# Optimization experiments

Hardware: AMD Instinct MI355X
Metric: run time of the kernel (lower is better)

The kernel has to match this reference:

```python
import jax, jax.numpy as jnp
import numpy as np

N = 200000
MESH = (128, 128, 128)   # mesh_dimensions
P = 4                    # spline_order
ALPHA = 0.35             # Ewald splitting parameter (1/Angstrom)
KE = 14.3996             # coulomb_constant, eV*A/e^2
BOX = 128.0              # cubic box edge, Angstrom


def _bspline(u, n):
    """Cardinal B-spline M_n(u), support [0, n]. Recursion depth = n-2 (static)."""
    if n == 2:
        return jnp.clip(1.0 - jnp.abs(u - 1.0), 0.0, 1.0)
    return (u * _bspline(u, n - 1) + (n - u) * _bspline(u - 1.0, n - 1)) / (n - 1)


def _spread_weights(frac_d, K):
    """Per-dimension P spline weights and wrapped grid indices for each atom."""
    u = frac_d * K
    base = jnp.floor(u)
    j = jnp.arange(P, dtype=frac_d.dtype)
    # evaluation points t_j = (u - base) + (P-1) - j, each in (0, P)
    t = (u - base)[:, None] + (P - 1) - j                      # [N, P]
    w = _bspline(t, P)                                         # [N, P]
    idx = (base.astype(jnp.int32)[:, None] - (P - 1)
           + jnp.arange(P, dtype=jnp.int32)) % K               # [N, P]
    return w, idx


def _bmod2(K):
    """|b(m)|^2 Euler exponential-spline factors for one mesh dimension."""
    m = (jnp.fft.fftfreq(K) * K).astype(jnp.float32)
    k = jnp.arange(P - 1, dtype=jnp.float32)
    Mv = _bspline(k + 1.0, P)                                  # M_P(1..P-1)
    D = (Mv[None, :] * jnp.exp(2j * jnp.pi * m[:, None] * k[None, :] / K)).sum(-1)
    return (1.0 / jnp.maximum(jnp.abs(D) ** 2, 1e-12)).astype(jnp.float32)


def _pme_energy(positions, charges, cell):
    Kx, Ky, Kz = MESH
    cellinv = jnp.linalg.inv(cell)
    V = jnp.abs(jnp.linalg.det(cell))
    frac = (positions @ cellinv) % 1.0                         # [N, 3]

    # --- B-spline charge spreading (scatter) ---
    wx, ix = _spread_weights(frac[:, 0], Kx)
    wy, iy = _spread_weights(frac[:, 1], Ky)
    wz, iz = _spread_weights(frac[:, 2], Kz)
    w3 = (charges[:, None, None, None]
          * wx[:, :, None, None] * wy[:, None, :, None] * wz[:, None, None, :])
    lin = (ix[:, :, None, None] * Ky + iy[:, None, :, None]) * Kz + iz[:, None, None, :]
    Q = (jnp.zeros(Kx * Ky * Kz, dtype=positions.dtype)
         .at[lin.reshape(-1)].add(w3.reshape(-1))
         .reshape(MESH))

    # --- reciprocal space ---
    S = jnp.fft.fftn(Q)
    S2 = (S * jnp.conj(S)).real                                # |F[Q]|^2
    b3 = (_bmod2(Kx)[:, None, None] * _bmod2(Ky)[None, :, None]
          * _bmod2(Kz)[None, None, :])
    mx = (jnp.fft.fftfreq(Kx) * Kx).astype(positions.dtype)
    my = (jnp.fft.fftfreq(Ky) * Ky).astype(positions.dtype)
    mz = (jnp.fft.fftfreq(Kz) * Kz).astype(positions.dtype)
    mg = jnp.stack(jnp.meshgrid(mx, my, mz, indexing='ij'), axis=-1)  # [Kx,Ky,Kz,3]
    kvec = 2.0 * jnp.pi * jnp.einsum('xyzm,nm->xyzn', mg, cellinv)
    k2 = (kvec ** 2).sum(-1)
    G = jnp.where(k2 > 0.0,
                  jnp.exp(-k2 / (4.0 * ALPHA ** 2)) / jnp.where(k2 > 0.0, k2, 1.0),
                  0.0)
    e_rec = KE * (2.0 * jnp.pi / V) * (G * b3 * S2).sum()
    e_self = -KE * ALPHA / jnp.sqrt(jnp.pi).astype(positions.dtype) * (charges ** 2).sum()
    return e_rec + e_self


def setup_inputs() -> dict:
    key = jax.random.key(0)
    k1, k2 = jax.random.split(key)
    positions = jax.random.uniform(k1, (N, 3), dtype=jnp.float32) * BOX
    charges = jax.random.normal(k2, (N,), dtype=jnp.float32) * 0.5
    charges = charges - charges.mean()   # neutral system (k=0 mode excluded)
    cell = jnp.eye(3, dtype=jnp.float32) * BOX
    return {"positions": positions, "charges": charges, "cell": cell}


def reference(positions, charges, cell):
    # energy [B=1, 1] and analytic forces [N, 3] via force gather (dE/dr)
    e, g = jax.value_and_grad(lambda p: _pme_energy(p, charges, cell))(positions)
    return (jnp.reshape(e, (1, 1)), -g)
```

## Files before the change

kernel.cpp:

```cpp
#include <hip/hip_runtime.h>

#define KDIM 128
#define NTOT (KDIM * KDIM * KDIM)
#define BPD 16
#define NBINS (BPD * BPD * BPD)
#define TILE_D 11
#define T2 (TILE_D * TILE_D)
#define TILE_N (TILE_D * TILE_D * TILE_D)
#define TPAD 1332
#define TSTRIDE 1344
#define CHUNK 256
#define NZKEEP 65
#define NSCALE_BLK (NZKEEP * 8)
#define ST 17
#define ZST 17

static constexpr float PI_F = 3.14159265358979323846f;
static constexpr float TWO_PI_F = 6.28318530717958647692f;
static constexpr float KE_F = 14.3996f;
static constexpr float ALPHA_F = 0.35f;

__device__ __forceinline__ int brev7(int i) { return (int)(__brev((unsigned)i) >> 25); }

__device__ __forceinline__ void inv3x3(const float* c, float* inv, float* adet) {
    float a00 = c[0], a01 = c[1], a02 = c[2];
    float a10 = c[3], a11 = c[4], a12 = c[5];
    float a20 = c[6], a21 = c[7], a22 = c[8];
    float det = a00 * (a11 * a22 - a12 * a21) - a01 * (a10 * a22 - a12 * a20) +
                a02 * (a10 * a21 - a11 * a20);
    float id = 1.0f / det;
    inv[0] = (a11 * a22 - a12 * a21) * id;
    inv[1] = (a02 * a21 - a01 * a22) * id;
    inv[2] = (a01 * a12 - a02 * a11) * id;
    inv[3] = (a12 * a20 - a10 * a22) * id;
    inv[4] = (a00 * a22 - a02 * a20) * id;
    inv[5] = (a02 * a10 - a00 * a12) * id;
    inv[6] = (a10 * a21 - a11 * a20) * id;
    inv[7] = (a01 * a20 - a00 * a21) * id;
    inv[8] = (a00 * a11 - a01 * a10) * id;
    *adet = fabsf(det);
}

__device__ __forceinline__ void bspline4(float f, float* w, float* dw) {
    float f2 = f * f, f3 = f2 * f;
    float omf = 1.0f - f;
    w[0] = omf * omf * omf * (1.0f / 6.0f);
    w[1] = (3.0f * f3 - 6.0f * f2 + 4.0f) * (1.0f / 6.0f);
    w[2] = (-3.0f * f3 + 3.0f * f2 + 3.0f * f + 1.0f) * (1.0f / 6.0f);
    w[3] = f3 * (1.0f / 6.0f);
    dw[0] = -0.5f * omf * omf;
    dw[1] = 1.5f * f2 - 2.0f * f;
    dw[2] = -1.5f * f2 + f + 0.5f;
    dw[3] = 0.5f * f2;
}

__device__ __forceinline__ void atom_base(const float* __restrict__ pos, const float* inv,
                                          int i, int base[3], float fpart[3]) {
    float p0 = pos[3 * i], p1 = pos[3 * i + 1], p2 = pos[3 * i + 2];
#pragma unroll
    for (int d = 0; d < 3; d++) {
        float fr = p0 * inv[d] + p1 * inv[3 + d] + p2 * inv[6 + d];
        fr -= floorf(fr);
        float u = fr * (float)KDIM;
        float bs = floorf(u);
        fpart[d] = u - bs;
        int b = (int)bs;
        base[d] = b & (KDIM - 1);
    }
}

__device__ __forceinline__ void atom_setup(const float* __restrict__ pos, const float* inv,
                                           int i, float wgt[3][4], float dwg[3][4],
                                           int idx[3][4]) {
    int base[3];
    float fp[3];
    atom_base(pos, inv, i, base, fp);
#pragma unroll
    for (int d = 0; d < 3; d++) {
        bspline4(fp[d], wgt[d], dwg[d]);
#pragma unroll
        for (int j = 0; j < 4; j++) idx[d][j] = (base[d] - 3 + j + KDIM) & (KDIM - 1);
    }
}

__device__ __forceinline__ float bmod2f(int x) {
    float th = (TWO_PI_F / (float)KDIM) * (float)x;
    float s1, c1, s2, c2;
    __sincosf(th, &s1, &c1);
    __sincosf(th + th, &s2, &c2);
    float dr = 0.16666667f + 0.66666667f * c1 + 0.16666667f * c2;
    float di = 0.66666667f * s1 + 0.16666667f * s2;
    float d2 = dr * dr + di * di;
    return 1.0f / fmaxf(d2, 1e-12f);
}

__global__ __launch_bounds__(256) void zero_tbl_kernel(int* __restrict__ counts,
                                                       int* __restrict__ cursor,
                                                       float* __restrict__ mtblS,
                                                       float* __restrict__ btblS) {
    int i = blockIdx.x * 256 + threadIdx.x;
    if (i < NBINS) {
        counts[i] = 0;
        cursor[i] = 0;
    }
    if (blockIdx.x == 0 && threadIdx.x < KDIM) {
        int r = brev7(threadIdx.x);
        mtblS[threadIdx.x] = (float)(r < 64 ? r : r - 128);
        btblS[threadIdx.x] = bmod2f(r);
    }
}

__global__ __launch_bounds__(256) void hist_kernel(const float* __restrict__ pos,
                                                   const float* __restrict__ chg,
                                                   const float* __restrict__ cell,
                                                   int* __restrict__ counts,
                                                   float* __restrict__ q2_part, int n) {
    __shared__ float hred[4];
    int i = blockIdx.x * blockDim.x + threadIdx.x;
    float q2 = 0.0f;
    if (i < n) {
        float inv[9], det;
        inv3x3(cell, inv, &det);
        int base[3];
        float fp[3];
        atom_base(pos, inv, i, base, fp);
        int bid = ((base[0] >> 3) << 8) | ((base[1] >> 3) << 4) | (base[2] >> 3);
        atomicAdd(&counts[bid], 1);
        float qi = chg[i];
        q2 = qi * qi;
    }
#pragma unroll
    for (int off = 32; off; off >>= 1) q2 += __shfl_down(q2, off);
    if ((threadIdx.x & 63) == 0) hred[threadIdx.x >> 6] = q2;
    __syncthreads();
    if (threadIdx.x == 0) q2_part[blockIdx.x] = hred[0] + hred[1] + hred[2] + hred[3];
}

__global__ __launch_bounds__(256) void scan_kernel(const int* __restrict__ counts,
                                                   int* __restrict__ starts) {
    __shared__ int part[256];
    int tid = threadIdx.x;
    int local[NBINS / 256];
    int sum = 0;
#pragma unroll
    for (int k = 0; k < NBINS / 256; k++) {
        local[k] = counts[tid * (NBINS / 256) + k];
        sum += local[k];
    }
    part[tid] = sum;
    __syncthreads();
    if (tid == 0) {
        int acc = 0;
        for (int i = 0; i < 256; i++) {
            int t = part[i];
            part[i] = acc;
            acc += t;
        }
        starts[NBINS] = acc;
    }
    __syncthreads();
    int acc = part[tid];
#pragma unroll
    for (int k = 0; k < NBINS / 256; k++) {
        starts[tid * (NBINS / 256) + k] = acc;
        acc += local[k];
    }
}

__global__ __launch_bounds__(256) void scatter_kernel(const float* __restrict__ pos,
                                                      const float* __restrict__ chg,
                                                      const float* __restrict__ cell,
                                                      const int* __restrict__ starts,
                                                      int* __restrict__ cursor,
                                                      float* __restrict__ records,
                                                      int* __restrict__ binatoms, int n) {
    int i = blockIdx.x * blockDim.x + threadIdx.x;
    if (i >= n) return;
    float inv[9], det;
    inv3x3(cell, inv, &det);
    int base[3];
    float fp[3];
    atom_base(pos, inv, i, base, fp);
    int bid = ((base[0] >> 3) << 8) | ((base[1] >> 3) << 4) | (base[2] >> 3);
    int slot = atomicAdd(&cursor[bid], 1) + starts[bid];
    binatoms[slot] = i;
    float4* rec = (float4*)(records + (size_t)slot * 16);
    float w[4], dw[4];
    float qi = chg[i];
    bspline4(fp[0], w, dw);
    rec[0] = make_float4(qi * w[0], qi * w[1], qi * w[2], qi * w[3]);
    bspline4(fp[1], w, dw);
    rec[1] = make_float4(w[0], w[1], w[2], w[3]);
    bspline4(fp[2], w, dw);
    rec[2] = make_float4(w[0], w[1], w[2], w[3]);
    int loc = (base[0] & 7) | ((base[1] & 7) << 4) | ((base[2] & 7) << 8);
    rec[3] = make_float4(__int_as_float(loc), 0.0f, 0.0f, 0.0f);
}

__global__ __launch_bounds__(256) void spread_bins_kernel(
    const float* __restrict__ records, const int* __restrict__ starts,
    float* __restrict__ tiles) {
    __shared__ float tile4[4 * TPAD];
    __shared__ float4 arec[CHUNK * 4];
    int tid = threadIdx.x;
    int bid = blockIdx.x;
    for (int i = tid; i < 4 * TPAD; i += 256) tile4[i] = 0.0f;
    int s = starts[bid], e = starts[bid + 1];
    int w = tid >> 6, l = tid & 63;
    int j0 = l >> 4, j1 = (l >> 2) & 3, j2 = l & 3;
    int joff = j0 * T2 + j1 * TILE_D + j2;
    float* mytile = tile4 + w * TPAD;
    for (int c0 = s; c0 < e; c0 += CHUNK) {
        int cnt = min(CHUNK, e - c0);
        __syncthreads();
        if (tid < cnt) {
            const float4* rp = (const float4*)records + (size_t)(c0 + tid) * 4;
            arec[tid * 4 + 0] = rp[0];
            arec[tid * 4 + 1] = rp[1];
            arec[tid * 4 + 2] = rp[2];
            arec[tid * 4 + 3] = rp[3];
        }
        __syncthreads();
        for (int a = w; a < cnt; a += 4) {
            const float* A = (const float*)&arec[a << 2];
            float val = A[j0] * A[4 + j1] * A[8 + j2];
            int lc = __float_as_int(A[12]);
            int tb = (lc & 15) * T2 + ((lc >> 4) & 15) * TILE_D + ((lc >> 8) & 15);
            mytile[tb + joff] += val;
        }
    }
    __syncthreads();
    float* tout = tiles + (size_t)bid * TSTRIDE;
    for (int i = tid; i < TILE_N; i += 256)
        tout[i] = tile4[i] + tile4[TPAD + i] + tile4[2 * TPAD + i] + tile4[3 * TPAD + i];
}

__device__ __forceinline__ float2 cmul(float2 a, float cs, float sn) {
    return make_float2(a.x * cs - a.y * sn, a.x * sn + a.y * cs);
}

__device__ __forceinline__ void wave_fft128_dif(float2& v0, float2& v1, int l, float sign) {
    {
        float ang = sign * (PI_F / 64.0f) * (float)l;
        float sn, cs;
        __sincosf(ang, &sn, &cs);
        float2 d = make_float2(v0.x - v1.x, v0.y - v1.y);
        v0 = make_float2(v0.x + v1.x, v0.y + v1.y);
        v1 = cmul(d, cs, sn);
    }
#pragma unroll
    for (int m = 32; m >= 1; m >>= 1) {
        float ang = sign * (PI_F / (float)m) * (float)(l & (m - 1));
        float sn, cs;
        __sincosf(ang, &sn, &cs);
        bool hi = (l & m) != 0;
        float2 p0, p1;
        p0.x = __shfl_xor(v0.x, m);
        p0.y = __shfl_xor(v0.y, m);
        p1.x = __shfl_xor(v1.x, m);
        p1.y = __shfl_xor(v1.y, m);
        float2 a0 = hi ? cmul(make_float2(p0.x - v0.x, p0.y - v0.y), cs, sn)
                       : make_float2(v0.x + p0.x, v0.y + p0.y);
        float2 a1 = hi ? cmul(make_float2(p1.x - v1.x, p1.y - v1.y), cs, sn)
                       : make_float2(v1.x + p1.x, v1.y + p1.y);
        v0 = a0;
        v1 = a1;
    }
}

__device__ __forceinline__ void wave_fft128_dit(float2& v0, float2& v1, int l, float sign) {
#pragma unroll
    for (int m = 1; m <= 32; m <<= 1) {
        float2 p0, p1;
        p0.x = __shfl_xor(v0.x, m);
        p0.y = __shfl_xor(v0.y, m);
        p1.x = __shfl_xor(v1.x, m);
        p1.y = __shfl_xor(v1.y, m);
        float ang = sign * (PI_F / (float)m) * (float)(l & (m - 1));
        float sn, cs;
        __sincosf(ang, &sn, &cs);
        bool hi = (l & m) != 0;
        float2 o0 = hi ? v0 : p0, e0 = hi ? p0 : v0;
        float2 o1 = hi ? v1 : p1, e1 = hi ? p1 : v1;
        float2 t0 = cmul(o0, cs, sn);
        float2 t1 = cmul(o1, cs, sn);
        float s = hi ? -1.0f : 1.0f;
        v0 = make_float2(e0.x + s * t0.x, e0.y + s * t0.y);
        v1 = make_float2(e1.x + s * t1.x, e1.y + s * t1.y);
    }
    float ang = sign * (PI_F / 64.0f) * (float)l;
    float sn, cs;
    __sincosf(ang, &sn, &cs);
    float2 t = cmul(v1, cs, sn);
    float2 e = v0;
    v0 = make_float2(e.x + t.x, e.y + t.y);
    v1 = make_float2(e.x - t.x, e.y - t.y);
}

__device__ __forceinline__ float merge_val(const float* __restrict__ tiles, int nx, int ny,
                                           const int* bxs, const int* lxs, const int* bys,
                                           const int* lys, int gz) {
    int bz = gz >> 3, oz = gz & 7;
    int nz = (oz >= 5) ? 2 : 1;
    int bzs[2] = {bz, (bz + 1) & 15}, lzs[2] = {oz + 3, oz - 5};
    float v = 0.0f;
    for (int i = 0; i < nx; i++)
        for (int j = 0; j < ny; j++) {
            int bxy = (bxs[i] << 8) | (bys[j] << 4);
            int lo = lxs[i] * T2 + lys[j] * TILE_D;
            for (int k = 0; k < nz; k++)
                v += tiles[(size_t)(bxy | bzs[k]) * TSTRIDE + lo + lzs[k]];
        }
    return v;
}

__global__ __launch_bounds__(512) void fft_z_merge(const float* __restrict__ tiles,
                                                   float2* __restrict__ C_t) {
    __shared__ float tr[128 * 9], ti[128 * 9];
    int w = threadIdx.x >> 6, l = threadIdx.x & 63;
    int line = (blockIdx.x << 3) + w;
    int gx = line >> 7, gy = line & 127;
    int bx = gx >> 3, ox = gx & 7;
    int by = gy >> 3, oy = gy & 7;
    int nx = (ox >= 5) ? 2 : 1, ny = (oy >= 5) ? 2 : 1;
    int bxs[2] = {bx, (bx + 1) & 15}, lxs[2] = {ox + 3, ox - 5};
    int bys[2] = {by, (by + 1) & 15}, lys[2] = {oy + 3, oy - 5};
    float m0 = merge_val(tiles, nx, ny, bxs, lxs, bys, lys, l);
    float m1 = merge_val(tiles, nx, ny, bxs, lxs, bys, lys, l + 64);
    tr[l * 9 + w] = m0;
    ti[l * 9 + w] = 0.0f;
    tr[(l + 64) * 9 + w] = m1;
    ti[(l + 64) * 9 + w] = 0.0f;
    int r = brev7(l);
    float2 v0 = make_float2(tr[r * 9 + w], 0.0f);
    float2 v1 = make_float2(tr[(r + 1) * 9 + w], 0.0f);
    wave_fft128_dit(v0, v1, l, -1.0f);
    tr[l * 9 + w] = v0.x;
    ti[l * 9 + w] = v0.y;
    tr[(l + 64) * 9 + w] = v1.x;
    ti[(l + 64) * 9 + w] = v1.y;
    __syncthreads();
    int xy0 = blockIdx.x << 3;
#pragma unroll
    for (int k = 0; k < 2; k++) {
        int e = threadIdx.x + (k << 9);
        int ss = e >> 3, wl = e & 7;
        if (ss < NZKEEP)
            C_t[(size_t)ss * (KDIM * KDIM) + xy0 + wl] =
                make_float2(tr[ss * 9 + wl], ti[ss * 9 + wl]);
    }
}

template <int DIF>
__global__ __launch_bounds__(512) void fft_y(float2* __restrict__ C_t) {
    int w = threadIdx.x >> 6, l = threadIdx.x & 63;
    int line = (blockIdx.x << 3) + w;
    int base = line << 7;
    float2 v0, v1;
    if (DIF) {
        v0 = C_t[base + l];
        v1 = C_t[base + l + 64];
        wave_fft128_dif(v0, v1, l, -1.0f);
    } else {
        int r = brev7(l);
        float4 f = ((const float4*)C_t)[(line << 6) + (r >> 1)];
        v0 = make_float2(f.x, f.y);
        v1 = make_float2(f.z, f.w);
        wave_fft128_dit(v0, v1, l, 1.0f);
    }
    C_t[base + l] = v0;
    C_t[base + l + 64] = v1;
}

__global__ __launch_bounds__(512) void fft_x_scale(float2* __restrict__ C_t,
                                                   const float* __restrict__ cell,
                                                   const float* __restrict__ mtblS,
                                                   const float* __restrict__ btblS,
                                                   float* __restrict__ scale_part) {
    __shared__ float2 lds[128 * ST];
    __shared__ float red[8];
    int tid = threadIdx.x;
    int s = blockIdx.x >> 3;
    int y0 = (blockIdx.x & 7) << 4;
    int base = s * (KDIM * KDIM) + y0;
#pragma unroll
    for (int k = 0; k < 2; k++) {
        int e = tid + (k << 9);
        int ll = e >> 3, zq = e & 7;
        float4 f = ((const float4*)C_t)[(base >> 1) + ll * 64 + zq];
        lds[ll * ST + 2 * zq] = make_float2(f.x, f.y);
        lds[ll * ST + 2 * zq + 1] = make_float2(f.z, f.w);
    }
    __syncthreads();
    int w = tid >> 6, l = tid & 63;
    float inv[9], det;
    inv3x3(cell, inv, &det);
    float mz = (s == 64) ? -64.0f : (float)s;
    float bz = bmod2f(s);
    float wz = (s == 0 || s == 64) ? 1.0f : 2.0f;
    float contrib = 0.0f;
#pragma unroll
    for (int c = 0; c < 2; c++) {
        int zt = (w << 1) | c;
        float2 v0 = lds[l * ST + zt];
        float2 v1 = lds[(l + 64) * ST + zt];
        wave_fft128_dif(v0, v1, l, -1.0f);
        int yp = y0 + zt;
        float my = mtblS[yp];
        float byz = btblS[yp] * bz;
#pragma unroll
        for (int h = 0; h < 2; h++) {
            int xs = l + (h << 6);
            float mx = mtblS[xs];
            float kx = TWO_PI_F * (mx * inv[0] + my * inv[1] + mz * inv[2]);
            float ky = TWO_PI_F * (mx * inv[3] + my * inv[4] + mz * inv[5]);
            float kz = TWO_PI_F * (mx * inv[6] + my * inv[7] + mz * inv[8]);
            float k2 = kx * kx + ky * ky + kz * kz;
            float A = 0.0f;
            if (k2 > 0.0f)
                A = __expf(-k2 / (4.0f * ALPHA_F * ALPHA_F)) / k2 * btblS[xs] * byz;
            float2& v = h ? v1 : v0;
            contrib += A * (v.x * v.x + v.y * v.y);
            v.x *= A;
            v.y *= A;
        }
        wave_fft128_dit(v0, v1, l, 1.0f);
        lds[l * ST + zt] = v0;
        lds[(l + 64) * ST + zt] = v1;
    }
    contrib *= wz;
#pragma unroll
    for (int off = 32; off; off >>= 1) contrib += __shfl_down(contrib, off);
    if (l == 0) red[w] = contrib;
    __syncthreads();
    if (tid == 0) {
        float v = 0.0f;
        for (int i = 0; i < 8; i++) v += red[i];
        scale_part[blockIdx.x] = v;
    }
#pragma unroll
    for (int k = 0; k < 2; k++) {
        int e = tid + (k << 9);
        int ll = e >> 3, zq = e & 7;
        float2 a = lds[ll * ST + 2 * zq];
        float2 b = lds[ll * ST + 2 * zq + 1];
        ((float4*)C_t)[(base >> 1) + ll * 64 + zq] = make_float4(a.x, a.y, b.x, b.y);
    }
}

__global__ __launch_bounds__(512) void fft_z_phi(const float2* __restrict__ C_t,
                                                 float* __restrict__ phi) {
    __shared__ float tr[NZKEEP * ZST], ti[NZKEEP * ZST];
    int tid = threadIdx.x;
    int xy0 = blockIdx.x << 4;
    for (int e = tid; e < NZKEEP * 16; e += 512) {
        int ss = e >> 4, q = e & 15;
        float2 v = C_t[(size_t)ss * (KDIM * KDIM) + xy0 + q];
        tr[ss * ZST + q] = v.x;
        ti[ss * ZST + q] = v.y;
    }
    __syncthreads();
    int w = tid >> 6, l = tid & 63;
    int r = brev7(l);
#pragma unroll
    for (int c0 = 0; c0 < 2; c0++) {
        int c = (w << 1) | c0;
        float2 v0, v1;
        if (r <= 62) {
            v0 = make_float2(tr[r * ZST + c], ti[r * ZST + c]);
            v1 = make_float2(tr[(r + 1) * ZST + c], ti[(r + 1) * ZST + c]);
        } else if (r == 64) {
            v0 = make_float2(tr[64 * ZST + c], ti[64 * ZST + c]);
            v1 = make_float2(tr[63 * ZST + c], -ti[63 * ZST + c]);
        } else {
            int m0 = 128 - r;
            v0 = make_float2(tr[m0 * ZST + c], -ti[m0 * ZST + c]);
            v1 = make_float2(tr[(m0 - 1) * ZST + c], -ti[(m0 - 1) * ZST + c]);
        }
        wave_fft128_dit(v0, v1, l, 1.0f);
        phi[(xy0 + c) * KDIM + l] = v0.x;
        phi[(xy0 + c) * KDIM + l + 64] = v1.x;
    }
}

__global__ __launch_bounds__(256) void finalize_kernel(const float* __restrict__ scale_part,
                                                       const float* __restrict__ q2_part,
                                                       int nq2,
                                                       const float* __restrict__ cell,
                                                       float* __restrict__ out) {
    __shared__ double sd[256];
    int tid = threadIdx.x;
    double es = 0.0;
    for (int i = tid; i < NSCALE_BLK; i += 256) es += (double)scale_part[i];
    double q2 = 0.0;
    for (int i = tid; i < nq2; i += 256) q2 += (double)q2_part[i];
    sd[tid] = es;
    __syncthreads();
    for (int s = 128; s; s >>= 1) {
        if (tid < s) sd[tid] += sd[tid + s];
        __syncthreads();
    }
    double esum = sd[0];
    __syncthreads();
    sd[tid] = q2;
    __syncthreads();
    for (int s = 128; s; s >>= 1) {
        if (tid < s) sd[tid] += sd[tid + s];
        __syncthreads();
    }
    if (tid == 0) {
        float inv[9], det;
        inv3x3(cell, inv, &det);
        double c = (double)KE_F * 2.0 * 3.14159265358979323846 / (double)det;
        double e = c * esum -
                   (double)KE_F * (double)ALPHA_F / 1.7724538509055160273 * sd[0];
        out[0] = (float)e;
    }
}

__global__ __launch_bounds__(256) void gather_kernel(const float* __restrict__ pos,
                                                     const float* __restrict__ chg,
                                                     const float* __restrict__ cell,
                                                     const int* __restrict__ binatoms,
                                                     const float* __restrict__ phi,
                                                     float* __restrict__ out, int n) {
    int a = blockIdx.x * blockDim.x + threadIdx.x;
    if (a >= n) return;
    int i = binatoms[a];
    float inv[9], det;
    inv3x3(cell, inv, &det);
    float wgt[3][4], dwg[3][4];
    int idx[3][4];
    atom_setup(pos, inv, i, wgt, dwg, idx);
    float acc0 = 0.0f, acc1 = 0.0f, acc2 = 0.0f;
#pragma unroll
    for (int j0 = 0; j0 < 4; j0++) {
        int r0 = idx[0][j0] << 14;
        float wx = wgt[0][j0], dx = dwg[0][j0];
#pragma unroll
        for (int j1 = 0; j1 < 4; j1++) {
            int r1 = r0 + (idx[1][j1] << 7);
            float wy = wgt[1][j1], dy = dwg[1][j1];
            float c00 = wx * wy;
            float c01 = wx * dy;
            float c02 = dx * wy;
#pragma unroll
            for (int j2 = 0; j2 < 4; j2++) {
                float p = phi[r1 + idx[2][j2]];
                float wz = wgt[2][j2], dz = dwg[2][j2];
                acc0 += p * c02 * wz;
                acc1 += p * c01 * wz;
                acc2 += p * c00 * dz;
            }
        }
    }
    float qi = chg[i];
    float c = KE_F * TWO_PI_F / det;
    float fac = -2.0f * c * qi * (float)KDIM;
    out[1 + 3 * i + 0] = fac * (acc0 * inv[0] + acc1 * inv[1] + acc2 * inv[2]);
    out[1 + 3 * i + 1] = fac * (acc0 * inv[3] + acc1 * inv[4] + acc2 * inv[5]);
    out[1 + 3 * i + 2] = fac * (acc0 * inv[6] + acc1 * inv[7] + acc2 * inv[8]);
}

extern "C" void kernel_launch(void* const* d_in, const int* in_sizes, int n_in,
                              void* d_out, int out_size, void* d_ws, size_t ws_size,
                              hipStream_t stream) {
    const float* pos = (const float*)d_in[0];
    const float* chg = (const float*)d_in[1];
    const float* cell = (const float*)d_in[2];
    float* out = (float*)d_out;
    int n = in_sizes[1];
    int nb = (n + 255) / 256;

    char* w = (char*)d_ws;
    float2* C_t = (float2*)w;
    size_t off = (size_t)NTOT * sizeof(float2);
    float* tiles = (float*)(w + off);
    off += (size_t)NBINS * TSTRIDE * sizeof(float);
    int* counts = (int*)(w + off);
    off += NBINS * sizeof(int);
    int* cursor = (int*)(w + off);
    off += NBINS * sizeof(int);
    int* starts = (int*)(w + off);
    off += (NBINS + 1) * sizeof(int);
    int* binatoms = (int*)(w + off);
    off += (size_t)n * sizeof(int);
    float* scale_part = (float*)(w + off);
    off += NSCALE_BLK * sizeof(float);
    float* q2_part = (float*)(w + off);
    off += (size_t)nb * sizeof(float);
    float* mtblS = (float*)(w + off);
    off += KDIM * sizeof(float);
    float* btblS = (float*)(w + off);

    float* records = (float*)C_t;
    float* phi = (float*)tiles;

    zero_tbl_kernel<<<(NBINS + 255) / 256, 256, 0, stream>>>(counts, cursor, mtblS, btblS);
    hist_kernel<<<nb, 256, 0, stream>>>(pos, chg, cell, counts, q2_part, n);
    scan_kernel<<<1, 256, 0, stream>>>(counts, starts);
    scatter_kernel<<<nb, 256, 0, stream>>>(pos, chg, cell, starts, cursor, records,
                                           binatoms, n);
    spread_bins_kernel<<<NBINS, 256, 0, stream>>>(records, starts, tiles);

    fft_z_merge<<<2048, 512, 0, stream>>>(tiles, C_t);
    fft_y<1><<<NZKEEP * KDIM / 8, 512, 0, stream>>>(C_t);
    fft_x_scale<<<NSCALE_BLK, 512, 0, stream>>>(C_t, cell, mtblS, btblS, scale_part);
    fft_y<0><<<NZKEEP * KDIM / 8, 512, 0, stream>>>(C_t);
    fft_z_phi<<<KDIM * KDIM / 16, 512, 0, stream>>>(C_t, phi);

    finalize_kernel<<<1, 256, 0, stream>>>(scale_part, q2_part, nb, cell, out);
    gather_kernel<<<nb, 256, 0, stream>>>(pos, chg, cell, binatoms, phi, out, n);
}
```

Baseline: 152.4 us.

## Shrink scatter records, recompute splines in spread, fuse finalize into gather

Scatter now writes compact 32-byte records (fractional parts, charge, local offset) instead of 64-byte precomputed weight records, and spread_bins recomputes the B-spline weights on load. The finalize energy reduction is folded into block 0 of the gather kernel, which removes one kernel launch. Gather now loads four contiguous z values per (x,y) with a 16-byte load when no z wraparound occurs and factors the z-sum. This trades less global record traffic and fewer launches for extra spline arithmetic and serial reduction work in one gather block.

```diff
diff --git a/kernel.cpp b/kernel.cpp
--- a/kernel.cpp
+++ b/kernel.cpp
@@ -21,6 +21,13 @@
 static constexpr float ALPHA_F = 0.35f;
 
 __device__ __forceinline__ int brev7(int i) { return (int)(__brev((unsigned)i) >> 25); }
+
+struct pf4 { float a, b, c, d; };
+__device__ __forceinline__ pf4 ld4u(const float* p) {
+    pf4 v;
+    __builtin_memcpy(&v, p, 16);
+    return v;
+}
 
 __device__ __forceinline__ void inv3x3(const float* c, float* inv, float* adet) {
     float a00 = c[0], a01 = c[1], a02 = c[2];
@@ -66,20 +73,6 @@
         fpart[d] = u - bs;
         int b = (int)bs;
         base[d] = b & (KDIM - 1);
-    }
-}
-
-__device__ __forceinline__ void atom_setup(const float* __restrict__ pos, const float* inv,
-                                           int i, float wgt[3][4], float dwg[3][4],
-                                           int idx[3][4]) {
-    int base[3];
-    float fp[3];
-    atom_base(pos, inv, i, base, fp);
-#pragma unroll
-    for (int d = 0; d < 3; d++) {
-        bspline4(fp[d], wgt[d], dwg[d]);
-#pragma unroll
-        for (int j = 0; j < 4; j++) idx[d][j] = (base[d] - 3 + j + KDIM) & (KDIM - 1);
     }
 }
 
@@ -184,17 +177,10 @@
     int bid = ((base[0] >> 3) << 8) | ((base[1] >> 3) << 4) | (base[2] >> 3);
     int slot = atomicAdd(&cursor[bid], 1) + starts[bid];
     binatoms[slot] = i;
-    float4* rec = (float4*)(records + (size_t)slot * 16);
-    float w[4], dw[4];
-    float qi = chg[i];
-    bspline4(fp[0], w, dw);
-    rec[0] = make_float4(qi * w[0], qi * w[1], qi * w[2], qi * w[3]);
-    bspline4(fp[1], w, dw);
-    rec[1] = make_float4(w[0], w[1], w[2], w[3]);
-    bspline4(fp[2], w, dw);
-    rec[2] = make_float4(w[0], w[1], w[2], w[3]);
     int loc = (base[0] & 7) | ((base[1] & 7) << 4) | ((base[2] & 7) << 8);
-    rec[3] = make_float4(__int_as_float(loc), 0.0f, 0.0f, 0.0f);
+    float4* rec = (float4*)(records + (size_t)slot * 8);
+    rec[0] = make_float4(fp[0], fp[1], fp[2], chg[i]);
+    rec[1] = make_float4(__int_as_float(loc), 0.0f, 0.0f, 0.0f);
 }
 
 __global__ __launch_bounds__(256) void spread_bins_kernel(
@@ -214,11 +200,18 @@
         int cnt = min(CHUNK, e - c0);
         __syncthreads();
         if (tid < cnt) {
-            const float4* rp = (const float4*)records + (size_t)(c0 + tid) * 4;
-            arec[tid * 4 + 0] = rp[0];
-            arec[tid * 4 + 1] = rp[1];
-            arec[tid * 4 + 2] = rp[2];
-            arec[tid * 4 + 3] = rp[3];
+            const float4* rp = (const float4*)records + (size_t)(c0 + tid) * 2;
+            float4 r0 = rp[0];
+            float4 r1 = rp[1];
+            float wv[4], dv[4];
+            bspline4(r0.x, wv, dv);
+            arec[tid * 4 + 0] =
+                make_float4(r0.w * wv[0], r0.w * wv[1], r0.w * wv[2], r0.w * wv[3]);
+            bspline4(r0.y, wv, dv);
+            arec[tid * 4 + 1] = make_float4(wv[0], wv[1], wv[2], wv[3]);
+            bspline4(r0.z, wv, dv);
+            arec[tid * 4 + 2] = make_float4(wv[0], wv[1], wv[2], wv[3]);
+            arec[tid * 4 + 3] = r1;
         }
         __syncthreads();
         for (int a = w; a < cnt; a += 4) {
@@ -483,74 +476,100 @@
     }
 }
 
-__global__ __launch_bounds__(256) void finalize_kernel(const float* __restrict__ scale_part,
-                                                       const float* __restrict__ q2_part,
-                                                       int nq2,
-                                                       const float* __restrict__ cell,
-                                                       float* __restrict__ out) {
+__global__ __launch_bounds__(256) void gather_kernel(
+    const float* __restrict__ pos, const float* __restrict__ chg,
+    const float* __restrict__ cell, const int* __restrict__ binatoms,
+    const float* __restrict__ phi, const float* __restrict__ scale_part,
+    const float* __restrict__ q2_part, int nq2, float* __restrict__ out, int n) {
     __shared__ double sd[256];
-    int tid = threadIdx.x;
-    double es = 0.0;
-    for (int i = tid; i < NSCALE_BLK; i += 256) es += (double)scale_part[i];
-    double q2 = 0.0;
-    for (int i = tid; i < nq2; i += 256) q2 += (double)q2_part[i];
-    sd[tid] = es;
-    __syncthreads();
-    for (int s = 128; s; s >>= 1) {
-        if (tid < s) sd[tid] += sd[tid + s];
+    if (blockIdx.x == 0) {
+        int tid = threadIdx.x;
+        double es = 0.0;
+        for (int i = tid; i < NSCALE_BLK; i += 256) es += (double)scale_part[i];
+        double q2 = 0.0;
+        for (int i = tid; i < nq2; i += 256) q2 += (double)q2_part[i];
+        sd[tid] = es;
         __syncthreads();
-    }
-    double esum = sd[0];
-    __syncthreads();
-    sd[tid] = q2;
-    __syncthreads();
-    for (int s = 128; s; s >>= 1) {
-        if (tid < s) sd[tid] += sd[tid + s];
+        for (int s = 128; s; s >>= 1) {
+            if (tid < s) sd[tid] += sd[tid + s];
+            __syncthreads();
+        }
+        double esum = sd[0];
         __syncthreads();
-    }
-    if (tid == 0) {
-        float inv[9], det;
-        inv3x3(cell, inv, &det);
-        double c = (double)KE_F * 2.0 * 3.14159265358979323846 / (double)det;
-        double e = c * esum -
-                   (double)KE_F * (double)ALPHA_F / 1.7724538509055160273 * sd[0];
-        out[0] = (float)e;
-    }
-}
-
-__global__ __launch_bounds__(256) void gather_kernel(const float* __restrict__ pos,
-                                                     const float* __restrict__ chg,
-                                                     const float* __restrict__ cell,
-                                                     const int* __restrict__ binatoms,
-                                                     const float* __restrict__ phi,
-                                                     float* __restrict__ out, int n) {
+        sd[tid] = q2;
+        __syncthreads();
+        for (int s = 128; s; s >>= 1) {
+            if (tid < s) sd[tid] += sd[tid + s];
+            __syncthreads();
+        }
+        if (tid == 0) {
+            float invf[9], det;
+            inv3x3(cell, invf, &det);
+            double cc = (double)KE_F * 2.0 * 3.14159265358979323846 / (double)det;
+            double e = cc * esum -
+                       (double)KE_F * (double)ALPHA_F / 1.7724538509055160273 * sd[0];
+            out[0] = (float)e;
+        }
+    }
     int a = blockIdx.x * blockDim.x + threadIdx.x;
     if (a >= n) return;
     int i = binatoms[a];
     float inv[9], det;
     inv3x3(cell, inv, &det);
-    float wgt[3][4], dwg[3][4];
-    int idx[3][4];
-    atom_setup(pos, inv, i, wgt, dwg, idx);
+    int base[3];
+    float fp[3];
+    atom_base(pos, inv, i, base, fp);
+    float wx[4], wy[4], wzv[4], dxv[4], dyv[4], dzv[4];
+    bspline4(fp[0], wx, dxv);
+    bspline4(fp[1], wy, dyv);
+    bspline4(fp[2], wzv, dzv);
+    int ix[4], iy[4];
+#pragma unroll
+    for (int j = 0; j < 4; j++) {
+        ix[j] = (base[0] - 3 + j + KDIM) & (KDIM - 1);
+        iy[j] = (base[1] - 3 + j + KDIM) & (KDIM - 1);
+    }
     float acc0 = 0.0f, acc1 = 0.0f, acc2 = 0.0f;
-#pragma unroll
-    for (int j0 = 0; j0 < 4; j0++) {
-        int r0 = idx[0][j0] << 14;
-        float wx = wgt[0][j0], dx = dwg[0][j0];
-#pragma unroll
-        for (int j1 = 0; j1 < 4; j1++) {
-            int r1 = r0 + (idx[1][j1] << 7);
-            float wy = wgt[1][j1], dy = dwg[1][j1];
-            float c00 = wx * wy;
-            float c01 = wx * dy;
-            float c02 = dx * wy;
-#pragma unroll
-            for (int j2 = 0; j2 < 4; j2++) {
-                float p = phi[r1 + idx[2][j2]];
-                float wz = wgt[2][j2], dz = dwg[2][j2];
-                acc0 += p * c02 * wz;
-                acc1 += p * c01 * wz;
-                acc2 += p * c00 * dz;
+    int bz = base[2];
+    if (bz >= 3) {
+        int z0 = bz - 3;
+#pragma unroll
+        for (int j0 = 0; j0 < 4; j0++) {
+            int r0 = ix[j0] << 14;
+            float wxx = wx[j0], dxx = dxv[j0];
+#pragma unroll
+            for (int j1 = 0; j1 < 4; j1++) {
+                pf4 p = ld4u(&phi[r0 + (iy[j1] << 7) + z0]);
+                float sw = p.a * wzv[0] + p.b * wzv[1] + p.c * wzv[2] + p.d * wzv[3];
+                float sdz = p.a * dzv[0] + p.b * dzv[1] + p.c * dzv[2] + p.d * dzv[3];
+                float wyy = wy[j1];
+                acc0 += sw * dxx * wyy;
+                acc1 += sw * wxx * dyv[j1];
+                acc2 += sdz * wxx * wyy;
+            }
+        }
+    } else {
+        int iz[4];
+#pragma unroll
+        for (int j = 0; j < 4; j++) iz[j] = (bz - 3 + j + KDIM) & (KDIM - 1);
+#pragma unroll
+        for (int j0 = 0; j0 < 4; j0++) {
+            int r0 = ix[j0] << 14;
+            float wxx = wx[j0], dxx = dxv[j0];
+#pragma unroll
+            for (int j1 = 0; j1 < 4; j1++) {
+                int r1 = r0 + (iy[j1] << 7);
+                float sw = 0.0f, sdz = 0.0f;
+#pragma unroll
+                for (int j2 = 0; j2 < 4; j2++) {
+                    float p = phi[r1 + iz[j2]];
+                    sw += p * wzv[j2];
+                    sdz += p * dzv[j2];
+                }
+                float wyy = wy[j1];
+                acc0 += sw * dxx * wyy;
+                acc1 += sw * wxx * dyv[j1];
+                acc2 += sdz * wxx * wyy;
             }
         }
     }
@@ -609,6 +628,6 @@
     fft_y<0><<<NZKEEP * KDIM / 8, 512, 0, stream>>>(C_t);
     fft_z_phi<<<KDIM * KDIM / 16, 512, 0, stream>>>(C_t, phi);
 
-    finalize_kernel<<<1, 256, 0, stream>>>(scale_part, q2_part, nb, cell, out);
-    gather_kernel<<<nb, 256, 0, stream>>>(pos, chg, cell, binatoms, phi, out, n);
-}
+    gather_kernel<<<nb, 256, 0, stream>>>(pos, chg, cell, binatoms, phi, scale_part,
+                                          q2_part, nb, out, n);
+}
```

Result: faster. 140.1 us (-8.0%).
